# Optimization experiments

Hardware: AMD Instinct MI355X
Metric: run time of the kernel (lower is better)

## Reference

```python
import jax, jax.numpy as jnp
import numpy as np

N = 50000
E = 800000
IN_DIM, HID, LAT, DEC_HID = 256, 256, 128, 512


def _glorot(key, shape):
    fan_in, fan_out = shape
    lim = np.sqrt(6.0 / (fan_in + fan_out))
    return jax.random.uniform(key, shape, jnp.float32, -lim, lim)


def setup_inputs() -> dict:
    key = jax.random.key(0)
    ks = jax.random.split(key, 10)
    x = jax.random.normal(ks[0], (N, IN_DIM), jnp.float32)
    edge_index = jax.random.randint(ks[1], (2, E), 0, N, dtype=jnp.int64)
    return {
        "x": x,
        "edge_index": edge_index,
        "W1": _glorot(ks[2], (IN_DIM, HID)), "b1": jnp.zeros((HID,), jnp.float32),
        "W2": _glorot(ks[3], (HID, LAT)), "b2": jnp.zeros((LAT,), jnp.float32),
        "Wd1": _glorot(ks[4], (LAT, DEC_HID)), "bd1": jnp.zeros((DEC_HID,), jnp.float32),
        "Wd2": _glorot(ks[5], (DEC_HID, IN_DIM)), "bd2": jnp.zeros((IN_DIM,), jnp.float32),
    }


def _gcn_layer(x, src, dst, W, b, num_nodes):
    # linear transform
    xt = x @ W + b                      # [N, out]
    # scatter-mean aggregation over incoming edges (PyG aggr='mean')
    msg = xt[src]                       # [E, out] gather of source features
    summed = jax.ops.segment_sum(msg, dst, num_segments=num_nodes)
    cnt = jax.ops.segment_sum(jnp.ones((src.shape[0],), xt.dtype), dst,
                              num_segments=num_nodes)
    mean = summed / jnp.maximum(cnt, 1.0)[:, None]   # 0 for isolated nodes
    # relu + residual
    return jax.nn.relu(mean) + xt


def reference(x, edge_index, W1, b1, W2, b2, Wd1, bd1, Wd2, bd2):
    src, dst = edge_index[0], edge_index[1]
    h = _gcn_layer(x, src, dst, W1, b1, x.shape[0])
    z = _gcn_layer(h, src, dst, W2, b2, x.shape[0])
    # decoder MLP
    x_hat = jax.nn.relu(z @ Wd1 + bd1) @ Wd2 + bd2
    return (x_hat, z)
```

## Files before the change

kernel.cpp:

```cpp
#include <hip/hip_runtime.h>
#include <hip/hip_bf16.h>

#define TPB 256

typedef __attribute__((ext_vector_type(8))) short short8;
typedef __attribute__((ext_vector_type(4))) float f32x4;

__device__ __forceinline__ unsigned short f2bf(float f) {
    unsigned int u = __float_as_uint(f);
    u = (u + 0x7FFFu + ((u >> 16) & 1u)) >> 16;
    return (unsigned short)u;
}
__device__ __forceinline__ float bflo(unsigned int u) { return __uint_as_float(u << 16); }
__device__ __forceinline__ float bfhi(unsigned int u) { return __uint_as_float(u & 0xFFFF0000u); }

__global__ void transpose_convert_all(
    const float* __restrict__ Wa, unsigned short* __restrict__ Ta, int Ka, int Na,
    const float* __restrict__ Wb, unsigned short* __restrict__ Tb, int Kb, int Nb,
    const float* __restrict__ Wc, unsigned short* __restrict__ Tc, int Kc, int Nc_,
    const float* __restrict__ Wd, unsigned short* __restrict__ Td, int Kd, int Nd)
{
    __shared__ float tile[32][33];
    int b = blockIdx.x;
    const float* W; unsigned short* T; int K, Nn;
    const int ta = (Na / 32) * (Ka / 32);
    const int tb = (Nb / 32) * (Kb / 32);
    const int tc = (Nc_ / 32) * (Kc / 32);
    if (b < ta)                { W = Wa; T = Ta; K = Ka; Nn = Na; }
    else if (b < ta + tb)      { b -= ta;           W = Wb; T = Tb; K = Kb; Nn = Nb; }
    else if (b < ta + tb + tc) { b -= ta + tb;      W = Wc; T = Tc; K = Kc; Nn = Nc_; }
    else                       { b -= ta + tb + tc; W = Wd; T = Td; K = Kd; Nn = Nd; }
    const int nx = Nn / 32;
    const int n0 = (b % nx) * 32;
    const int k0 = (b / nx) * 32;
    const int tx = threadIdx.x, ty = threadIdx.y;
#pragma unroll
    for (int i = 0; i < 4; ++i)
        tile[ty + i * 8][tx] = W[(size_t)(k0 + ty + i * 8) * Nn + n0 + tx];
    __syncthreads();
#pragma unroll
    for (int i = 0; i < 4; ++i)
        T[(size_t)(n0 + ty + i * 8) * K + k0 + tx] = f2bf(tile[tx][ty + i * 8]);
}

struct ARegsBF {
    short8 v[2];
    __device__ __forceinline__ void load(const unsigned short* A, int K, int bm,
                                         int sr, int c8, int k0, int M) {
#pragma unroll
        for (int i = 0; i < 2; ++i) {
            const int gm = bm + sr + i * 32;
            v[i] = (gm < M) ? *reinterpret_cast<const short8*>(A + (size_t)gm * K + k0 + c8 * 8)
                            : (short8)0;
        }
    }
    __device__ __forceinline__ short8 get(int i) const { return v[i]; }
};
struct ARegsF32 {
    float4 v[2][2];
    __device__ __forceinline__ void load(const float* A, int K, int bm,
                                         int sr, int c8, int k0, int M) {
#pragma unroll
        for (int i = 0; i < 2; ++i) {
            const int gm = bm + sr + i * 32;
            if (gm < M) {
                const float* p = A + (size_t)gm * K + k0 + c8 * 8;
                v[i][0] = *reinterpret_cast<const float4*>(p);
                v[i][1] = *reinterpret_cast<const float4*>(p + 4);
            } else {
                v[i][0] = make_float4(0.f, 0.f, 0.f, 0.f);
                v[i][1] = make_float4(0.f, 0.f, 0.f, 0.f);
            }
        }
    }
    __device__ __forceinline__ short8 get(int i) const {
        short8 r;
        r[0] = (short)f2bf(v[i][0].x); r[1] = (short)f2bf(v[i][0].y);
        r[2] = (short)f2bf(v[i][0].z); r[3] = (short)f2bf(v[i][0].w);
        r[4] = (short)f2bf(v[i][1].x); r[5] = (short)f2bf(v[i][1].y);
        r[6] = (short)f2bf(v[i][1].z); r[7] = (short)f2bf(v[i][1].w);
        return r;
    }
};
template <typename TA> struct ASel;
template <> struct ASel<float>          { using type = ARegsF32; };
template <> struct ASel<unsigned short> { using type = ARegsBF;  };

__device__ __forceinline__ void copy_out(unsigned short* C, const float* Cst, const float* bias,
                                         int bm, int bn, int M, int Nc, int t, bool doRelu) {
#pragma unroll
    for (int it = 0; it < 4; ++it) {
        const int idx = it * 2048 + t * 8;
        const int row = idx >> 7, col = idx & 127;
        const int m = bm + row;
        if (m >= M) continue;
        float4 v0 = *reinterpret_cast<const float4*>(&Cst[idx]);
        float4 v1 = *reinterpret_cast<const float4*>(&Cst[idx + 4]);
        float4 b0 = *reinterpret_cast<const float4*>(&bias[bn + col]);
        float4 b1 = *reinterpret_cast<const float4*>(&bias[bn + col + 4]);
        float o[8] = {v0.x + b0.x, v0.y + b0.y, v0.z + b0.z, v0.w + b0.w,
                      v1.x + b1.x, v1.y + b1.y, v1.z + b1.z, v1.w + b1.w};
        short8 s;
#pragma unroll
        for (int j = 0; j < 8; ++j) {
            const float vv = doRelu ? fmaxf(o[j], 0.f) : o[j];
            s[j] = (short)f2bf(vv);
        }
        *reinterpret_cast<short8*>(&C[(size_t)m * Nc + bn + col]) = s;
    }
}
__device__ __forceinline__ void copy_out(float* C, const float* Cst, const float* bias,
                                         int bm, int bn, int M, int Nc, int t, bool doRelu) {
#pragma unroll
    for (int it = 0; it < 8; ++it) {
        const int idx = it * 1024 + t * 4;
        const int row = idx >> 7, col = idx & 127;
        const int m = bm + row;
        if (m >= M) continue;
        float4 v = *reinterpret_cast<const float4*>(&Cst[idx]);
        float4 b = *reinterpret_cast<const float4*>(&bias[bn + col]);
        v.x += b.x; v.y += b.y; v.z += b.z; v.w += b.w;
        if (doRelu) {
            v.x = fmaxf(v.x, 0.f); v.y = fmaxf(v.y, 0.f);
            v.z = fmaxf(v.z, 0.f); v.w = fmaxf(v.w, 0.f);
        }
        *reinterpret_cast<float4*>(&C[(size_t)m * Nc + bn + col]) = v;
    }
}

template <typename TA, typename TC, bool RELU>
__global__ __launch_bounds__(256) void mfma_gemm_kernel(
    const TA* __restrict__ A, const unsigned short* __restrict__ Bt,
    const float* __restrict__ bias, TC* __restrict__ C,
    int M, int Nc, int K)
{
    __shared__ unsigned short lds_s[16384];

    const int t  = threadIdx.x;
    const int l  = t & 63;
    const int w  = t >> 6;
    const int wm = w >> 1, wn = w & 1;
    const int bm = blockIdx.x * 64;
    const int bn = blockIdx.y * 128;

    const int sr = t >> 3;
    const int c8 = t & 7;

    f32x4 acc[2][4] = {};

    typename ASel<TA>::type ar;
    short8 br[4];

    auto loadB = [&](int k0) {
#pragma unroll
        for (int i = 0; i < 4; ++i) {
            const int rb = sr + i * 32;
            br[i] = *reinterpret_cast<const short8*>(Bt + (size_t)(bn + rb) * K + k0 + c8 * 8);
        }
    };
    auto writeTiles = [&]() {
#pragma unroll
        for (int i = 0; i < 2; ++i) {
            const int r = sr + i * 32;
            const int slot = c8 ^ (r & 7);
            *reinterpret_cast<short8*>(&lds_s[r * 64 + slot * 8]) = ar.get(i);
        }
#pragma unroll
        for (int i = 0; i < 4; ++i) {
            const int r = sr + i * 32;
            const int slot = c8 ^ (r & 7);
            *reinterpret_cast<short8*>(&lds_s[4096 + r * 64 + slot * 8]) = br[i];
        }
    };

    ar.load(A, K, bm, sr, c8, 0, M);
    loadB(0);
    writeTiles();
    __syncthreads();

    for (int k0 = 0; k0 < K; k0 += 64) {
        const bool nxt = (k0 + 64) < K;
        if (nxt) {
            ar.load(A, K, bm, sr, c8, k0 + 64, M);
            loadB(k0 + 64);
        }

#pragma unroll
        for (int kk = 0; kk < 2; ++kk) {
            short8 af[2], bf4[4];
#pragma unroll
            for (int mf = 0; mf < 2; ++mf) {
                const int row  = wm * 32 + mf * 16 + (l & 15);
                const int slot = (kk * 4 + (l >> 4)) ^ (row & 7);
                af[mf] = *reinterpret_cast<const short8*>(&lds_s[row * 64 + slot * 8]);
            }
#pragma unroll
            for (int nf = 0; nf < 4; ++nf) {
                const int row  = wn * 64 + nf * 16 + (l & 15);
                const int slot = (kk * 4 + (l >> 4)) ^ (row & 7);
                bf4[nf] = *reinterpret_cast<const short8*>(&lds_s[4096 + row * 64 + slot * 8]);
            }
#pragma unroll
            for (int mf = 0; mf < 2; ++mf)
#pragma unroll
                for (int nf = 0; nf < 4; ++nf)
                    acc[mf][nf] = __builtin_amdgcn_mfma_f32_16x16x32_bf16(
                        af[mf], bf4[nf], acc[mf][nf], 0, 0, 0);
        }
        __syncthreads();
        if (nxt) { writeTiles(); __syncthreads(); }
    }

    float* Cst = reinterpret_cast<float*>(lds_s);
#pragma unroll
    for (int mf = 0; mf < 2; ++mf)
#pragma unroll
        for (int nf = 0; nf < 4; ++nf)
#pragma unroll
            for (int rr = 0; rr < 4; ++rr) {
                const int row = wm * 32 + mf * 16 + (l >> 4) * 4 + rr;
                const int col = wn * 64 + nf * 16 + (l & 15);
                Cst[row * 128 + col] = acc[mf][nf][rr];
            }
    __syncthreads();
    copy_out(C, Cst, bias, bm, bn, M, Nc, t, RELU);
}

__global__ void hist_kernel(const int* __restrict__ dst, int* __restrict__ counts, int E)
{
    int e = blockIdx.x * TPB + threadIdx.x;
    if (e < E) atomicAdd(&counts[dst[e]], 1);
}

__global__ void scan1_kernel(const int* __restrict__ counts,
                             int* __restrict__ local, int* __restrict__ bsum, int N)
{
    __shared__ int sh[TPB];
    const int t = threadIdx.x;
    const int base = blockIdx.x * 1024 + t * 4;
    int v[4];
#pragma unroll
    for (int i = 0; i < 4; ++i) v[i] = (base + i < N) ? counts[base + i] : 0;
    const int s = v[0] + v[1] + v[2] + v[3];
    sh[t] = s;
    __syncthreads();
    for (int d = 1; d < TPB; d <<= 1) {
        int x = (t >= d) ? sh[t - d] : 0;
        __syncthreads();
        sh[t] += x;
        __syncthreads();
    }
    int run = sh[t] - s;
#pragma unroll
    for (int i = 0; i < 4; ++i) {
        if (base + i < N) local[base + i] = run;
        run += v[i];
    }
    if (t == TPB - 1) bsum[blockIdx.x] = sh[TPB - 1];
}

__global__ void scan2_kernel(int* __restrict__ bsum, int nb)
{
    __shared__ int sh[TPB];
    const int t = threadIdx.x;
    const int v = (t < nb) ? bsum[t] : 0;
    sh[t] = v;
    __syncthreads();
    for (int d = 1; d < TPB; d <<= 1) {
        int x = (t >= d) ? sh[t - d] : 0;
        __syncthreads();
        sh[t] += x;
        __syncthreads();
    }
    if (t < nb) bsum[t] = sh[t] - v;
}

__global__ void scan3_kernel(int* __restrict__ offsets, int* __restrict__ cursor,
                             const int* __restrict__ bsum, int N)
{
    const int i = blockIdx.x * TPB + threadIdx.x;
    if (i < N) {
        const int o = offsets[i] + bsum[i >> 10];
        offsets[i] = o;
        cursor[i]  = o;
    }
}

__global__ void build_perm_kernel(const int* __restrict__ src, const int* __restrict__ dst,
                                  int* __restrict__ cursor, int* __restrict__ perm, int E)
{
    int e = blockIdx.x * TPB + threadIdx.x;
    if (e < E) {
        int pos = atomicAdd(&cursor[dst[e]], 1);
        perm[pos] = src[e];
    }
}

template <int F, int CH, bool WRITE_ZF32>
__global__ __launch_bounds__(256) void agg_kernel(
    const uint2* __restrict__ xt,
    const int* __restrict__ offsets, const int* __restrict__ counts,
    const int* __restrict__ perm,
    uint2* __restrict__ out, float* __restrict__ zf32, int N)
{
    constexpr int RU  = F / 4;
    constexpr int L   = RU / CH;
    constexpr int NPB = TPB / L;

    const int chunk = blockIdx.x % CH;
    const int node  = (blockIdx.x / CH) * NPB + threadIdx.x / L;
    const int g     = threadIdx.x % L;
    if (node >= N) return;
    const int col = chunk * L + g;

    const int start = offsets[node];
    const int deg   = counts[node];

    float a0 = 0.f, a1 = 0.f, a2 = 0.f, a3 = 0.f;

    for (int base = 0; base < deg; base += L) {
        const int m = min(L, deg - base);
        const int pidx = perm[start + base + ((g < m) ? g : (m - 1))];
        int j = 0;
        for (; j + 4 <= m; j += 4) {
            const int s0 = __shfl(pidx, j + 0, L);
            const int s1 = __shfl(pidx, j + 1, L);
            const int s2 = __shfl(pidx, j + 2, L);
            const int s3 = __shfl(pidx, j + 3, L);
            const uint2 v0 = xt[(size_t)s0 * RU + col];
            const uint2 v1 = xt[(size_t)s1 * RU + col];
            const uint2 v2 = xt[(size_t)s2 * RU + col];
            const uint2 v3 = xt[(size_t)s3 * RU + col];
            a0 += bflo(v0.x) + bflo(v1.x) + bflo(v2.x) + bflo(v3.x);
            a1 += bfhi(v0.x) + bfhi(v1.x) + bfhi(v2.x) + bfhi(v3.x);
            a2 += bflo(v0.y) + bflo(v1.y) + bflo(v2.y) + bflo(v3.y);
            a3 += bfhi(v0.y) + bfhi(v1.y) + bfhi(v2.y) + bfhi(v3.y);
        }
        for (; j < m; ++j) {
            const int s = __shfl(pidx, j, L);
            const uint2 v = xt[(size_t)s * RU + col];
            a0 += bflo(v.x); a1 += bfhi(v.x);
            a2 += bflo(v.y); a3 += bfhi(v.y);
        }
    }

    const float c = (float)max(deg, 1);
    const uint2 xv = xt[(size_t)node * RU + col];
    const float r0 = fmaxf(a0 / c, 0.f) + bflo(xv.x);
    const float r1 = fmaxf(a1 / c, 0.f) + bfhi(xv.x);
    const float r2 = fmaxf(a2 / c, 0.f) + bflo(xv.y);
    const float r3 = fmaxf(a3 / c, 0.f) + bfhi(xv.y);

    uint2 o;
    o.x = (unsigned int)f2bf(r0) | ((unsigned int)f2bf(r1) << 16);
    o.y = (unsigned int)f2bf(r2) | ((unsigned int)f2bf(r3) << 16);
    out[(size_t)node * RU + col] = o;
    if (WRITE_ZF32) {
        float4 z4 = make_float4(r0, r1, r2, r3);
        *reinterpret_cast<float4*>(&zf32[(size_t)node * F + 4 * col]) = z4;
    }
}

extern "C" void kernel_launch(void* const* d_in, const int* in_sizes, int n_in,
                              void* d_out, int out_size, void* d_ws, size_t ws_size,
                              hipStream_t stream)
{
    const int IN_DIM = 256, HID = 256, LAT = 128, DEC_HID = 512;
    const int N = in_sizes[0] / IN_DIM;
    const int E = in_sizes[1] / 2;

    const float* x   = (const float*)d_in[0];
    const int*   ei  = (const int*)d_in[1];
    const float* W1  = (const float*)d_in[2];
    const float* b1  = (const float*)d_in[3];
    const float* W2  = (const float*)d_in[4];
    const float* b2  = (const float*)d_in[5];
    const float* Wd1 = (const float*)d_in[6];
    const float* bd1 = (const float*)d_in[7];
    const float* Wd2 = (const float*)d_in[8];
    const float* bd2 = (const float*)d_in[9];

    const int* src = ei;
    const int* dst = ei + E;

    unsigned short* xt1  = (unsigned short*)d_ws;
    unsigned short* h    = xt1  + (size_t)N * 256;
    unsigned short* xt2  = h    + (size_t)N * 256;
    unsigned short* zbf  = xt2  + (size_t)N * 128;
    unsigned short* hdec = zbf  + (size_t)N * 128;
    unsigned short* wt1  = hdec + (size_t)N * 512;
    unsigned short* wt2  = wt1  + 256 * 256;
    unsigned short* wtd1 = wt2  + 128 * 256;
    unsigned short* wtd2 = wtd1 + 512 * 128;
    int* counts  = (int*)(wtd2 + 256 * 512);
    int* offsets = counts + N;
    int* cursor  = offsets + N;
    int* bsum    = cursor + N;
    int* perm    = bsum + 256;

    float* out_xhat = (float*)d_out;
    float* out_z    = out_xhat + (size_t)N * IN_DIM;

    dim3 blk(TPB);
    const int egrid = (E + TPB - 1) / TPB;
    const int mb64 = (N + 63) / 64;
    const int nscan = (N + 1023) / 1024;

    {
        const int tiles = (HID/32)*(IN_DIM/32) + (LAT/32)*(HID/32)
                        + (DEC_HID/32)*(LAT/32) + (IN_DIM/32)*(DEC_HID/32);
        transpose_convert_all<<<tiles, dim3(32, 8), 0, stream>>>(
            W1, wt1, IN_DIM, HID,  W2, wt2, HID, LAT,
            Wd1, wtd1, LAT, DEC_HID,  Wd2, wtd2, DEC_HID, IN_DIM);
    }

    hipMemsetAsync(counts, 0, (size_t)N * 4, stream);
    hist_kernel<<<egrid, blk, 0, stream>>>(dst, counts, E);
    scan1_kernel<<<nscan, blk, 0, stream>>>(counts, offsets, bsum, N);
    scan2_kernel<<<1, blk, 0, stream>>>(bsum, nscan);
    scan3_kernel<<<(N + TPB - 1) / TPB, blk, 0, stream>>>(offsets, cursor, bsum, N);
    build_perm_kernel<<<egrid, blk, 0, stream>>>(src, dst, cursor, perm, E);

    mfma_gemm_kernel<float, unsigned short, false><<<dim3(mb64, HID / 128), blk, 0, stream>>>(
        x, wt1, b1, xt1, N, HID, IN_DIM);
    {
        const int ngroups = (N + 15) / 16;
        agg_kernel<256, 4, false><<<ngroups * 4, blk, 0, stream>>>(
            (const uint2*)xt1, offsets, counts, perm, (uint2*)h, nullptr, N);
    }

    mfma_gemm_kernel<unsigned short, unsigned short, false><<<dim3(mb64, LAT / 128), blk, 0, stream>>>(
        h, wt2, b2, xt2, N, LAT, HID);
    {
        const int ngroups = (N + 7) / 8;
        agg_kernel<128, 1, true><<<ngroups, blk, 0, stream>>>(
            (const uint2*)xt2, offsets, counts, perm, (uint2*)zbf, out_z, N);
    }

    mfma_gemm_kernel<unsigned short, unsigned short, true><<<dim3(mb64, DEC_HID / 128), blk, 0, stream>>>(
        zbf, wtd1, bd1, hdec, N, DEC_HID, LAT);
    mfma_gemm_kernel<unsigned short, float, false><<<dim3(mb64, IN_DIM / 128), blk, 0, stream>>>(
        hdec, wtd2, bd2, out_xhat, N, IN_DIM, DEC_HID);
}
```

Measured before the change: 288.5 us.

## Load GEMM B fragments directly from global memory and double-buffer A in LDS

Restructures the MFMA GEMM so the weight (B) fragments are read straight from global/L2 into registers instead of being staged through LDS. Only the A tile goes through LDS, now double-buffered, which removes one barrier per K-step. K becomes a template parameter so the K loop unrolls fully. The epilogue stages the output in two 32-row halves to fit the smaller 16 KB LDS footprint, which may raise occupancy. The trade-off is uncoalesced, repeated B reads per wave that rely on cache hits.

```diff
diff --git a/kernel.cpp b/kernel.cpp
--- a/kernel.cpp
+++ b/kernel.cpp
@@ -43,56 +43,32 @@
         T[(size_t)(n0 + ty + i * 8) * K + k0 + tx] = f2bf(tile[tx][ty + i * 8]);
 }
 
-struct ARegsBF {
-    short8 v[2];
-    __device__ __forceinline__ void load(const unsigned short* A, int K, int bm,
-                                         int sr, int c8, int k0, int M) {
-#pragma unroll
-        for (int i = 0; i < 2; ++i) {
-            const int gm = bm + sr + i * 32;
-            v[i] = (gm < M) ? *reinterpret_cast<const short8*>(A + (size_t)gm * K + k0 + c8 * 8)
-                            : (short8)0;
-        }
-    }
-    __device__ __forceinline__ short8 get(int i) const { return v[i]; }
-};
-struct ARegsF32 {
-    float4 v[2][2];
-    __device__ __forceinline__ void load(const float* A, int K, int bm,
-                                         int sr, int c8, int k0, int M) {
-#pragma unroll
-        for (int i = 0; i < 2; ++i) {
-            const int gm = bm + sr + i * 32;
-            if (gm < M) {
-                const float* p = A + (size_t)gm * K + k0 + c8 * 8;
-                v[i][0] = *reinterpret_cast<const float4*>(p);
-                v[i][1] = *reinterpret_cast<const float4*>(p + 4);
-            } else {
-                v[i][0] = make_float4(0.f, 0.f, 0.f, 0.f);
-                v[i][1] = make_float4(0.f, 0.f, 0.f, 0.f);
-            }
-        }
-    }
-    __device__ __forceinline__ short8 get(int i) const {
-        short8 r;
-        r[0] = (short)f2bf(v[i][0].x); r[1] = (short)f2bf(v[i][0].y);
-        r[2] = (short)f2bf(v[i][0].z); r[3] = (short)f2bf(v[i][0].w);
-        r[4] = (short)f2bf(v[i][1].x); r[5] = (short)f2bf(v[i][1].y);
-        r[6] = (short)f2bf(v[i][1].z); r[7] = (short)f2bf(v[i][1].w);
-        return r;
-    }
-};
-template <typename TA> struct ASel;
-template <> struct ASel<float>          { using type = ARegsF32; };
-template <> struct ASel<unsigned short> { using type = ARegsBF;  };
-
-__device__ __forceinline__ void copy_out(unsigned short* C, const float* Cst, const float* bias,
-                                         int bm, int bn, int M, int Nc, int t, bool doRelu) {
-#pragma unroll
-    for (int it = 0; it < 4; ++it) {
+__device__ __forceinline__ void load_a16(const float* p, short8& lo, short8& hi) {
+    float4 f0 = *reinterpret_cast<const float4*>(p);
+    float4 f1 = *reinterpret_cast<const float4*>(p + 4);
+    float4 f2 = *reinterpret_cast<const float4*>(p + 8);
+    float4 f3 = *reinterpret_cast<const float4*>(p + 12);
+    lo[0] = (short)f2bf(f0.x); lo[1] = (short)f2bf(f0.y);
+    lo[2] = (short)f2bf(f0.z); lo[3] = (short)f2bf(f0.w);
+    lo[4] = (short)f2bf(f1.x); lo[5] = (short)f2bf(f1.y);
+    lo[6] = (short)f2bf(f1.z); lo[7] = (short)f2bf(f1.w);
+    hi[0] = (short)f2bf(f2.x); hi[1] = (short)f2bf(f2.y);
+    hi[2] = (short)f2bf(f2.z); hi[3] = (short)f2bf(f2.w);
+    hi[4] = (short)f2bf(f3.x); hi[5] = (short)f2bf(f3.y);
+    hi[6] = (short)f2bf(f3.z); hi[7] = (short)f2bf(f3.w);
+}
+__device__ __forceinline__ void load_a16(const unsigned short* p, short8& lo, short8& hi) {
+    lo = *reinterpret_cast<const short8*>(p);
+    hi = *reinterpret_cast<const short8*>(p + 8);
+}
+
+__device__ __forceinline__ void copy_out32(unsigned short* C, const float* Cst, const float* bias,
+                                           int rowbase, int bn, int M, int Nc, int t, bool doRelu) {
+#pragma unroll
+    for (int it = 0; it < 2; ++it) {
         const int idx = it * 2048 + t * 8;
         const int row = idx >> 7, col = idx & 127;
-        const int m = bm + row;
+        const int m = rowbase + row;
         if (m >= M) continue;
         float4 v0 = *reinterpret_cast<const float4*>(&Cst[idx]);
         float4 v1 = *reinterpret_cast<const float4*>(&Cst[idx + 4]);
@@ -109,13 +85,13 @@
         *reinterpret_cast<short8*>(&C[(size_t)m * Nc + bn + col]) = s;
     }
 }
-__device__ __forceinline__ void copy_out(float* C, const float* Cst, const float* bias,
-                                         int bm, int bn, int M, int Nc, int t, bool doRelu) {
-#pragma unroll
-    for (int it = 0; it < 8; ++it) {
+__device__ __forceinline__ void copy_out32(float* C, const float* Cst, const float* bias,
+                                           int rowbase, int bn, int M, int Nc, int t, bool doRelu) {
+#pragma unroll
+    for (int it = 0; it < 4; ++it) {
         const int idx = it * 1024 + t * 4;
         const int row = idx >> 7, col = idx & 127;
-        const int m = bm + row;
+        const int m = rowbase + row;
         if (m >= M) continue;
         float4 v = *reinterpret_cast<const float4*>(&Cst[idx]);
         float4 b = *reinterpret_cast<const float4*>(&bias[bn + col]);
@@ -128,13 +104,12 @@
     }
 }
 
-template <typename TA, typename TC, bool RELU>
-__global__ __launch_bounds__(256) void mfma_gemm_kernel(
+template <typename TA, typename TC, int K, bool RELU>
+__global__ __launch_bounds__(256) void mfma_gemm2(
     const TA* __restrict__ A, const unsigned short* __restrict__ Bt,
-    const float* __restrict__ bias, TC* __restrict__ C,
-    int M, int Nc, int K)
-{
-    __shared__ unsigned short lds_s[16384];
+    const float* __restrict__ bias, TC* __restrict__ C, int M, int Nc)
+{
+    __shared__ unsigned short lds_s[2][4096];
 
     const int t  = threadIdx.x;
     const int l  = t & 63;
@@ -143,87 +118,89 @@
     const int bm = blockIdx.x * 64;
     const int bn = blockIdx.y * 128;
 
-    const int sr = t >> 3;
-    const int c8 = t & 7;
+    const int r  = t >> 2;
+    const int q  = t & 3;
+    const int gm = bm + r;
+
+    const unsigned short* bbase = Bt + (size_t)(bn + wn * 64 + (l & 15)) * K + ((l >> 4) * 8);
 
     f32x4 acc[2][4] = {};
-
-    typename ASel<TA>::type ar;
-    short8 br[4];
-
-    auto loadB = [&](int k0) {
-#pragma unroll
-        for (int i = 0; i < 4; ++i) {
-            const int rb = sr + i * 32;
-            br[i] = *reinterpret_cast<const short8*>(Bt + (size_t)(bn + rb) * K + k0 + c8 * 8);
-        }
+    short8 sa0, sa1;
+
+    auto loadA = [&](int k0) {
+        if (gm < M) load_a16(A + (size_t)gm * K + k0 + q * 16, sa0, sa1);
+        else { sa0 = (short8)0; sa1 = (short8)0; }
     };
-    auto writeTiles = [&]() {
-#pragma unroll
-        for (int i = 0; i < 2; ++i) {
-            const int r = sr + i * 32;
-            const int slot = c8 ^ (r & 7);
-            *reinterpret_cast<short8*>(&lds_s[r * 64 + slot * 8]) = ar.get(i);
-        }
-#pragma unroll
-        for (int i = 0; i < 4; ++i) {
-            const int r = sr + i * 32;
-            const int slot = c8 ^ (r & 7);
-            *reinterpret_cast<short8*>(&lds_s[4096 + r * 64 + slot * 8]) = br[i];
-        }
+    auto writeA = [&](int buf) {
+        const int s0 = (q * 2)     ^ (r & 7);
+        const int s1 = (q * 2 + 1) ^ (r & 7);
+        *reinterpret_cast<short8*>(&lds_s[buf][r * 64 + s0 * 8]) = sa0;
+        *reinterpret_cast<short8*>(&lds_s[buf][r * 64 + s1 * 8]) = sa1;
     };
 
-    ar.load(A, K, bm, sr, c8, 0, M);
-    loadB(0);
-    writeTiles();
+    loadA(0);
+    writeA(0);
     __syncthreads();
 
-    for (int k0 = 0; k0 < K; k0 += 64) {
-        const bool nxt = (k0 + 64) < K;
-        if (nxt) {
-            ar.load(A, K, bm, sr, c8, k0 + 64, M);
-            loadB(k0 + 64);
-        }
+    int cur = 0;
+    constexpr int S = K / 64;
+#pragma unroll
+    for (int step = 0; step < S; ++step) {
+        const int k0 = step * 64;
+        if (step + 1 < S) loadA(k0 + 64);
+
+        short8 bf[2][4];
+#pragma unroll
+        for (int kk = 0; kk < 2; ++kk)
+#pragma unroll
+            for (int nf = 0; nf < 4; ++nf)
+                bf[kk][nf] = *reinterpret_cast<const short8*>(
+                    bbase + (size_t)nf * 16 * K + k0 + kk * 32);
 
 #pragma unroll
         for (int kk = 0; kk < 2; ++kk) {
-            short8 af[2], bf4[4];
+            short8 af[2];
 #pragma unroll
             for (int mf = 0; mf < 2; ++mf) {
                 const int row  = wm * 32 + mf * 16 + (l & 15);
                 const int slot = (kk * 4 + (l >> 4)) ^ (row & 7);
-                af[mf] = *reinterpret_cast<const short8*>(&lds_s[row * 64 + slot * 8]);
-            }
-#pragma unroll
-            for (int nf = 0; nf < 4; ++nf) {
-                const int row  = wn * 64 + nf * 16 + (l & 15);
-                const int slot = (kk * 4 + (l >> 4)) ^ (row & 7);
-                bf4[nf] = *reinterpret_cast<const short8*>(&lds_s[4096 + row * 64 + slot * 8]);
+                af[mf] = *reinterpret_cast<const short8*>(&lds_s[cur][row * 64 + slot * 8]);
             }
 #pragma unroll
             for (int mf = 0; mf < 2; ++mf)
 #pragma unroll
                 for (int nf = 0; nf < 4; ++nf)
                     acc[mf][nf] = __builtin_amdgcn_mfma_f32_16x16x32_bf16(
-                        af[mf], bf4[nf], acc[mf][nf], 0, 0, 0);
+                        af[mf], bf[kk][nf], acc[mf][nf], 0, 0, 0);
+        }
+
+        if (step + 1 < S) {
+            writeA(cur ^ 1);
+            __syncthreads();
+            cur ^= 1;
+        }
+    }
+
+    __syncthreads();
+    float* Cst = reinterpret_cast<float*>(lds_s);
+#pragma unroll
+    for (int p = 0; p < 2; ++p) {
+        if (wm == p) {
+#pragma unroll
+            for (int mf = 0; mf < 2; ++mf)
+#pragma unroll
+                for (int nf = 0; nf < 4; ++nf)
+#pragma unroll
+                    for (int rr = 0; rr < 4; ++rr) {
+                        const int row = mf * 16 + (l >> 4) * 4 + rr;
+                        const int col = wn * 64 + nf * 16 + (l & 15);
+                        Cst[row * 128 + col] = acc[mf][nf][rr];
+                    }
         }
         __syncthreads();
-        if (nxt) { writeTiles(); __syncthreads(); }
-    }
-
-    float* Cst = reinterpret_cast<float*>(lds_s);
-#pragma unroll
-    for (int mf = 0; mf < 2; ++mf)
-#pragma unroll
-        for (int nf = 0; nf < 4; ++nf)
-#pragma unroll
-            for (int rr = 0; rr < 4; ++rr) {
-                const int row = wm * 32 + mf * 16 + (l >> 4) * 4 + rr;
-                const int col = wn * 64 + nf * 16 + (l & 15);
-                Cst[row * 128 + col] = acc[mf][nf][rr];
-            }
-    __syncthreads();
-    copy_out(C, Cst, bias, bm, bn, M, Nc, t, RELU);
+        copy_out32(C, Cst, bias, bm + p * 32, bn, M, Nc, t, RELU);
+        if (p == 0) __syncthreads();
+    }
 }
 
 __global__ void hist_kernel(const int* __restrict__ dst, int* __restrict__ counts, int E)
@@ -421,24 +398,24 @@
     scan3_kernel<<<(N + TPB - 1) / TPB, blk, 0, stream>>>(offsets, cursor, bsum, N);
     build_perm_kernel<<<egrid, blk, 0, stream>>>(src, dst, cursor, perm, E);
 
-    mfma_gemm_kernel<float, unsigned short, false><<<dim3(mb64, HID / 128), blk, 0, stream>>>(
-        x, wt1, b1, xt1, N, HID, IN_DIM);
+    mfma_gemm2<float, unsigned short, 256, false><<<dim3(mb64, HID / 128), blk, 0, stream>>>(
+        x, wt1, b1, xt1, N, HID);
     {
         const int ngroups = (N + 15) / 16;
         agg_kernel<256, 4, false><<<ngroups * 4, blk, 0, stream>>>(
             (const uint2*)xt1, offsets, counts, perm, (uint2*)h, nullptr, N);
     }
 
-    mfma_gemm_kernel<unsigned short, unsigned short, false><<<dim3(mb64, LAT / 128), blk, 0, stream>>>(
-        h, wt2, b2, xt2, N, LAT, HID);
+    mfma_gemm2<unsigned short, unsigned short, 256, false><<<dim3(mb64, LAT / 128), blk, 0, stream>>>(
+        h, wt2, b2, xt2, N, LAT);
     {
         const int ngroups = (N + 7) / 8;
         agg_kernel<128, 1, true><<<ngroups, blk, 0, stream>>>(
             (const uint2*)xt2, offsets, counts, perm, (uint2*)zbf, out_z, N);
     }
 
-    mfma_gemm_kernel<unsigned short, unsigned short, true><<<dim3(mb64, DEC_HID / 128), blk, 0, stream>>>(
-        zbf, wtd1, bd1, hdec, N, DEC_HID, LAT);
-    mfma_gemm_kernel<unsigned short, float, false><<<dim3(mb64, IN_DIM / 128), blk, 0, stream>>>(
-        hdec, wtd2, bd2, out_xhat, N, IN_DIM, DEC_HID);
-}
+    mfma_gemm2<unsigned short, unsigned short, 128, true><<<dim3(mb64, DEC_HID / 128), blk, 0, stream>>>(
+        zbf, wtd1, bd1, hdec, N, DEC_HID);
+    mfma_gemm2<unsigned short, float, 512, false><<<dim3(mb64, IN_DIM / 128), blk, 0, stream>>>(
+        hdec, wtd2, bd2, out_xhat, N, IN_DIM);
+}
```

Result: slower. 343.7 us (+19.1%).
